# Optimization experiments

Measured on AMD Instinct MI355X. Metric: run time of the kernel, lower is better.

## Reference

```python
import jax, jax.numpy as jnp
import numpy as np

N = 100000        # nodes
E = 1600000       # edges (before self loops)
F_IN = 14         # Mutagenicity num_node_features
H = 64            # hidden_channels
C = 2             # Mutagenicity num_classes
G = 512           # graphs in batch
NEG_SLOPE = 0.2   # GATConv default leaky slope for attention logits


def setup_inputs() -> dict:
    key = jax.random.key(0)
    ks = jax.random.split(key, 40)
    inp = {
        "x": jax.random.normal(ks[0], (N, F_IN), jnp.float32),
        "edge_index": jax.random.randint(ks[1], (2, E), 0, N, dtype=jnp.int64),
        "batch": jnp.sort(jax.random.randint(ks[2], (N,), 0, G, dtype=jnp.int64)),
    }
    dims = [F_IN, H, H, H, H]
    ki = 3
    for l in range(5):
        fin = dims[l]
        s = 1.0 / np.sqrt(fin)
        inp[f"W{l}"] = jax.random.uniform(ks[ki], (fin, H), jnp.float32, -s, s); ki += 1
        inp[f"a_src{l}"] = jax.random.uniform(ks[ki], (H,), jnp.float32, -0.3, 0.3); ki += 1
        inp[f"a_dst{l}"] = jax.random.uniform(ks[ki], (H,), jnp.float32, -0.3, 0.3); ki += 1
        inp[f"b{l}"] = jnp.zeros((H,), jnp.float32)
    s = 1.0 / np.sqrt(H)
    inp["lin_W"] = jax.random.uniform(ks[ki], (H, C), jnp.float32, -s, s); ki += 1
    inp["lin_b"] = jnp.zeros((C,), jnp.float32)
    return inp


def _gat_layer(x, src, dst, W, a_s, a_d, b):
    # GATConv (heads=1): h = x W; e_ij = LeakyReLU(a_s.h_j + a_d.h_i);
    # alpha = softmax over incoming edges of node i; out_i = sum_j alpha_ij h_j + b
    h = x @ W                                   # [N, H]
    logit_s = h @ a_s                           # [N]
    logit_d = h @ a_d                           # [N]
    e = jax.nn.leaky_relu(logit_s[src] + logit_d[dst], NEG_SLOPE)  # [Etot]
    m = jax.ops.segment_max(e, dst, num_segments=N)
    m = jnp.where(jnp.isfinite(m), m, 0.0)      # empty segments -> 0 (none after self loops)
    ex = jnp.exp(e - m[dst])
    den = jax.ops.segment_sum(ex, dst, num_segments=N)
    alpha = ex / den[dst]                       # self loops guarantee den > 0
    out = jax.ops.segment_sum(alpha[:, None] * h[src], dst, num_segments=N)
    return out + b


def reference(x, edge_index, batch,
              W0, a_src0, a_dst0, b0,
              W1, a_src1, a_dst1, b1,
              W2, a_src2, a_dst2, b2,
              W3, a_src3, a_dst3, b3,
              W4, a_src4, a_dst4, b4,
              lin_W, lin_b):
    # add self loops once (GATConv default add_self_loops=True)
    loop = jnp.arange(N, dtype=edge_index.dtype)
    src = jnp.concatenate([edge_index[0], loop])
    dst = jnp.concatenate([edge_index[1], loop])

    h = x
    layers = [(W0, a_src0, a_dst0, b0), (W1, a_src1, a_dst1, b1),
              (W2, a_src2, a_dst2, b2), (W3, a_src3, a_dst3, b3),
              (W4, a_src4, a_dst4, b4)]
    for (W, a_s, a_d, b) in layers:
        h = jax.nn.elu(_gat_layer(h, src, dst, W, a_s, a_d, b))

    # global max pool over graphs
    g = jax.ops.segment_max(h, batch, num_segments=G)   # [G, H]
    g = jnp.where(jnp.isfinite(g), g, 0.0)
    return g @ lin_W + lin_b                             # [G, C]
```

## Files before the change

kernel.cpp:

```cpp
#include <hip/hip_runtime.h>
#include <hip/hip_fp16.h>
#include <math.h>

#define N_NODES 100000
#define H_DIM 64
#define G_GRAPHS 512
#define NEG_SLOPE 0.2f

#define BSHIFT 9
#define NBKT ((N_NODES + (1 << BSHIFT) - 1) >> BSHIFT)
#define CHUNK_E 4096

#define DEG_CAP 128

#define PK_SRC(v)  ((v) & 0x1FFFF)
#define PK_LD(v)   ((v) >> 17)


__global__ __launch_bounds__(256) void bucket_hist_kernel(const int* __restrict__ dst,
                                                          int* __restrict__ bcount, int E) {
    __shared__ int lh[NBKT];
    int t = threadIdx.x;
    for (int i = t; i < NBKT; i += 256) lh[i] = 0;
    __syncthreads();
    int base = blockIdx.x * CHUNK_E;
#pragma unroll
    for (int k = 0; k < 16; ++k) {
        int e = base + k * 256 + t;
        if (e < E) atomicAdd(&lh[dst[e] >> BSHIFT], 1);
    }
    __syncthreads();
    for (int i = t; i < NBKT; i += 256) {
        int c = lh[i];
        if (c) atomicAdd(&bcount[i], c);
    }
}

__global__ __launch_bounds__(256) void bucket_scan_kernel(const int* __restrict__ bcount,
                                                          int* __restrict__ bbase,
                                                          int* __restrict__ bfill,
                                                          int* __restrict__ off, int n) {
    __shared__ int sm[256];
    int t = threadIdx.x;
    sm[t] = (t < NBKT) ? bcount[t] : 0;
    __syncthreads();
    for (int d = 1; d < 256; d <<= 1) {
        int v = (t >= d) ? sm[t - d] : 0;
        __syncthreads();
        sm[t] += v;
        __syncthreads();
    }
    if (t < NBKT) {
        int ex = (t == 0) ? 0 : sm[t - 1];
        bbase[t] = ex;
        bfill[t] = ex;
    }
    if (t == 0) {
        bbase[NBKT] = sm[255];
        off[n] = sm[255];
    }
}

__global__ __launch_bounds__(256) void partition_kernel(const int* __restrict__ src,
                                                        const int* __restrict__ dst,
                                                        int* __restrict__ bfill,
                                                        int* __restrict__ ebuck, int E) {
    __shared__ int lh[NBKT];
    __shared__ int lbase[NBKT];
    int t = threadIdx.x;
    int base = blockIdx.x * CHUNK_E;
    for (int i = t; i < NBKT; i += 256) lh[i] = 0;
    __syncthreads();

    int pk[16], bk[16];
#pragma unroll
    for (int k = 0; k < 16; ++k) {
        int e = base + k * 256 + t;
        if (e < E) {
            int s = src[e];
            int d = dst[e];
            bk[k] = d >> BSHIFT;
            pk[k] = s | ((d & ((1 << BSHIFT) - 1)) << 17);
            atomicAdd(&lh[bk[k]], 1);
        } else {
            bk[k] = -1;
        }
    }
    __syncthreads();
    for (int i = t; i < NBKT; i += 256) {
        int c = lh[i];
        lbase[i] = c ? atomicAdd(&bfill[i], c) : 0;
        lh[i] = 0;
    }
    __syncthreads();
#pragma unroll
    for (int k = 0; k < 16; ++k) {
        if (bk[k] >= 0) {
            int r = atomicAdd(&lh[bk[k]], 1);
            ebuck[lbase[bk[k]] + r] = pk[k];
        }
    }
}

__global__ __launch_bounds__(256) void bucket_csr_kernel(const int* __restrict__ ebuck,
                                                         const int* __restrict__ bbase,
                                                         int* __restrict__ off,
                                                         int* __restrict__ esrc, int n) {
    __shared__ int cnt[512];
    __shared__ int loff[512];
    __shared__ int sm[256];
    int b = blockIdx.x;
    int t = threadIdx.x;
    int ebeg = bbase[b];
    int eend = bbase[b + 1];
    int nbeg = b << BSHIFT;
    int nloc = n - nbeg; if (nloc > 512) nloc = 512;

    cnt[t] = 0; cnt[t + 256] = 0;
    __syncthreads();
    for (int e = ebeg + t; e < eend; e += 256) {
        atomicAdd(&cnt[PK_LD(ebuck[e])], 1);
    }
    __syncthreads();
    int c0 = cnt[2 * t], c1 = cnt[2 * t + 1];
    sm[t] = c0 + c1;
    __syncthreads();
    for (int d = 1; d < 256; d <<= 1) {
        int v = (t >= d) ? sm[t - d] : 0;
        __syncthreads();
        sm[t] += v;
        __syncthreads();
    }
    int basep = (t == 0) ? 0 : sm[t - 1];
    loff[2 * t] = basep;
    loff[2 * t + 1] = basep + c0;
    cnt[2 * t] = 0; cnt[2 * t + 1] = 0;
    __syncthreads();
    for (int i = t; i < nloc; i += 256) off[nbeg + i] = ebeg + loff[i];
    for (int e = ebeg + t; e < eend; e += 256) {
        int v = ebuck[e];
        int d = PK_LD(v);
        int r = atomicAdd(&cnt[d], 1);
        esrc[ebeg + loff[d] + r] = PK_SRC(v);
    }
}

template <int FIN, int FINP, int XSTR>
__global__ __launch_bounds__(256) void gemm_tile_kernel(
        const float* __restrict__ act, const float* __restrict__ W,
        const float* __restrict__ a_s, const float* __restrict__ a_d,
        __half* __restrict__ h16,
        float* __restrict__ ls, float* __restrict__ ld,
        int n) {
    __shared__ float sx[128 * XSTR];
    __shared__ float sw[FINP * 64];
    int t = threadIdx.x;
    int tb = blockIdx.x * 128;
    int nrow = n - tb; if (nrow > 128) nrow = 128;

    {
        const float4* Wv = (const float4*)W;
        float4* swv = (float4*)sw;
        for (int i = t; i < FINP * 16; i += 256) {
            int k = i >> 4;
            swv[i] = (k < FIN) ? Wv[i] : make_float4(0.0f, 0.0f, 0.0f, 0.0f);
        }
    }
    if (FIN == 64) {
        for (int i = t; i < 128 * 16; i += 256) {
            int r = i >> 4, c4 = i & 15;
            float4 v = make_float4(0.0f, 0.0f, 0.0f, 0.0f);
            if (r < nrow) v = *(const float4*)(act + (size_t)(tb + r) * 64 + c4 * 4);
            *(float4*)(sx + r * XSTR + c4 * 4) = v;
        }
    } else {
        int c = t & 15;
        for (int r = t >> 4; r < 128; r += 16) {
            float v = 0.0f;
            if (r < nrow && c < FIN) v = act[(size_t)(tb + r) * FIN + c];
            sx[r * XSTR + c] = v;
        }
    }
    __syncthreads();

    int f4 = t & 15;
    int ng = t >> 4;

    float4 acc[8];
#pragma unroll
    for (int i = 0; i < 8; ++i) acc[i] = make_float4(0.0f, 0.0f, 0.0f, 0.0f);

    for (int k4 = 0; k4 < FINP; k4 += 4) {
        float4 w0 = *(const float4*)(sw + (k4 + 0) * 64 + f4 * 4);
        float4 w1 = *(const float4*)(sw + (k4 + 1) * 64 + f4 * 4);
        float4 w2 = *(const float4*)(sw + (k4 + 2) * 64 + f4 * 4);
        float4 w3 = *(const float4*)(sw + (k4 + 3) * 64 + f4 * 4);
#pragma unroll
        for (int i = 0; i < 8; ++i) {
            float4 xv = *(const float4*)(sx + (ng + 16 * i) * XSTR + k4);
            acc[i].x = fmaf(xv.x, w0.x, acc[i].x);
            acc[i].y = fmaf(xv.x, w0.y, acc[i].y);
            acc[i].z = fmaf(xv.x, w0.z, acc[i].z);
            acc[i].w = fmaf(xv.x, w0.w, acc[i].w);
            acc[i].x = fmaf(xv.y, w1.x, acc[i].x);
            acc[i].y = fmaf(xv.y, w1.y, acc[i].y);
            acc[i].z = fmaf(xv.y, w1.z, acc[i].z);
            acc[i].w = fmaf(xv.y, w1.w, acc[i].w);
            acc[i].x = fmaf(xv.z, w2.x, acc[i].x);
            acc[i].y = fmaf(xv.z, w2.y, acc[i].y);
            acc[i].z = fmaf(xv.z, w2.z, acc[i].z);
            acc[i].w = fmaf(xv.z, w2.w, acc[i].w);
            acc[i].x = fmaf(xv.w, w3.x, acc[i].x);
            acc[i].y = fmaf(xv.w, w3.y, acc[i].y);
            acc[i].z = fmaf(xv.w, w3.z, acc[i].z);
            acc[i].w = fmaf(xv.w, w3.w, acc[i].w);
        }
    }

    float4 as4 = *(const float4*)(a_s + f4 * 4);
    float4 ad4 = *(const float4*)(a_d + f4 * 4);
#pragma unroll
    for (int i = 0; i < 8; ++i) {
        int r = ng + 16 * i;
        if (r < nrow) {
            int node = tb + r;
            __half2 plo = __floats2half2_rn(acc[i].x, acc[i].y);
            __half2 phi = __floats2half2_rn(acc[i].z, acc[i].w);
            uint2 pk;
            pk.x = *reinterpret_cast<unsigned*>(&plo);
            pk.y = *reinterpret_cast<unsigned*>(&phi);
            *reinterpret_cast<uint2*>(h16 + (size_t)node * 64 + f4 * 4) = pk;
            float vs = acc[i].x * as4.x + acc[i].y * as4.y +
                       acc[i].z * as4.z + acc[i].w * as4.w;
            float vd = acc[i].x * ad4.x + acc[i].y * ad4.y +
                       acc[i].z * ad4.z + acc[i].w * ad4.w;
            vs += __shfl_xor(vs, 1, 64); vd += __shfl_xor(vd, 1, 64);
            vs += __shfl_xor(vs, 2, 64); vd += __shfl_xor(vd, 2, 64);
            vs += __shfl_xor(vs, 4, 64); vd += __shfl_xor(vd, 4, 64);
            vs += __shfl_xor(vs, 8, 64); vd += __shfl_xor(vd, 8, 64);
            if (f4 == 0) { ls[node] = vs; ld[node] = vd; }
        }
    }
}

__global__ __launch_bounds__(256) void gat_aggregate_kernel(
        const __half* __restrict__ h16,
        const float* __restrict__ ls,
        const float* __restrict__ ld, const int* __restrict__ off,
        const int* __restrict__ esrc, const float* __restrict__ bias,
        float* __restrict__ hout, int n) {
    __shared__ int2 smq[16 * DEG_CAP];
    int t = threadIdx.x;
    int fl = t & 15;
    int g = t >> 4;
    int node = blockIdx.x * 16 + g;
    if (node >= n) return;
    int2* sq = smq + g * DEG_CAP;
    int fl4 = fl * 4;

    int jb = off[node];
    int je = off[node + 1];
    int deg = je - jb;
    int degc = (deg < DEG_CAP) ? deg : DEG_CAP;
    float ldv = ld[node];
    float lself = ls[node];

    float mm = lself;
    for (int c = fl; c < degc; c += 16) {
        int s = esrc[jb + c];
        float v = ls[s];
        sq[c] = make_int2(s, __float_as_int(v));
        mm = fmaxf(mm, v);
    }
    for (int c = degc + fl; c < deg; c += 16) {
        mm = fmaxf(mm, ls[esrc[jb + c]]);
    }
    mm = fmaxf(mm, __shfl_xor(mm, 8, 64));
    mm = fmaxf(mm, __shfl_xor(mm, 4, 64));
    mm = fmaxf(mm, __shfl_xor(mm, 2, 64));
    mm = fmaxf(mm, __shfl_xor(mm, 1, 64));
    float mraw = mm + ldv;
    float m = (mraw >= 0.0f) ? mraw : NEG_SLOPE * mraw;

    float denl = 0.0f;
    for (int c = fl; c < degc; c += 16) {
        float e = __int_as_float(sq[c].y) + ldv;
        e = (e >= 0.0f) ? e : NEG_SLOPE * e;
        float p = __expf(e - m);
        sq[c].y = __float_as_int(p);
        denl += p;
    }
    int degc4 = (degc + 3) & ~3;
    if (fl < degc4 - degc) sq[degc + fl] = make_int2(node, 0);

    denl += __shfl_xor(denl, 8, 64);
    denl += __shfl_xor(denl, 4, 64);
    denl += __shfl_xor(denl, 2, 64);
    denl += __shfl_xor(denl, 1, 64);

    uint2 qs = *reinterpret_cast<const uint2*>(h16 + (size_t)node * 64 + fl4);
    float2 sa = __half22float2(*reinterpret_cast<__half2*>(&qs.x));
    float2 sb = __half22float2(*reinterpret_cast<__half2*>(&qs.y));

    float4 acc = make_float4(0.0f, 0.0f, 0.0f, 0.0f);
    for (int c = 0; c < degc4; c += 4) {
        int2 e0 = sq[c + 0];
        int2 e1 = sq[c + 1];
        int2 e2 = sq[c + 2];
        int2 e3 = sq[c + 3];
        uint2 q0 = *reinterpret_cast<const uint2*>(h16 + (size_t)e0.x * 64 + fl4);
        uint2 q1 = *reinterpret_cast<const uint2*>(h16 + (size_t)e1.x * 64 + fl4);
        uint2 q2 = *reinterpret_cast<const uint2*>(h16 + (size_t)e2.x * 64 + fl4);
        uint2 q3 = *reinterpret_cast<const uint2*>(h16 + (size_t)e3.x * 64 + fl4);
        float p0 = __int_as_float(e0.y), p1 = __int_as_float(e1.y);
        float p2 = __int_as_float(e2.y), p3 = __int_as_float(e3.y);
        float2 a0 = __half22float2(*reinterpret_cast<__half2*>(&q0.x));
        float2 b0 = __half22float2(*reinterpret_cast<__half2*>(&q0.y));
        float2 a1 = __half22float2(*reinterpret_cast<__half2*>(&q1.x));
        float2 b1 = __half22float2(*reinterpret_cast<__half2*>(&q1.y));
        float2 a2 = __half22float2(*reinterpret_cast<__half2*>(&q2.x));
        float2 b2 = __half22float2(*reinterpret_cast<__half2*>(&q2.y));
        float2 a3 = __half22float2(*reinterpret_cast<__half2*>(&q3.x));
        float2 b3 = __half22float2(*reinterpret_cast<__half2*>(&q3.y));
        acc.x = fmaf(p0, a0.x, acc.x); acc.y = fmaf(p0, a0.y, acc.y);
        acc.z = fmaf(p0, b0.x, acc.z); acc.w = fmaf(p0, b0.y, acc.w);
        acc.x = fmaf(p1, a1.x, acc.x); acc.y = fmaf(p1, a1.y, acc.y);
        acc.z = fmaf(p1, b1.x, acc.z); acc.w = fmaf(p1, b1.y, acc.w);
        acc.x = fmaf(p2, a2.x, acc.x); acc.y = fmaf(p2, a2.y, acc.y);
        acc.z = fmaf(p2, b2.x, acc.z); acc.w = fmaf(p2, b2.y, acc.w);
        acc.x = fmaf(p3, a3.x, acc.x); acc.y = fmaf(p3, a3.y, acc.y);
        acc.z = fmaf(p3, b3.x, acc.z); acc.w = fmaf(p3, b3.y, acc.w);
    }

    float den_of = 0.0f;
    for (int j = jb + DEG_CAP; j < je; ++j) {
        int s = esrc[j];
        float e = ls[s] + ldv;
        e = (e >= 0.0f) ? e : NEG_SLOPE * e;
        float p = __expf(e - m);
        den_of += p;
        uint2 qv = *reinterpret_cast<const uint2*>(h16 + (size_t)s * 64 + fl4);
        float2 va = __half22float2(*reinterpret_cast<__half2*>(&qv.x));
        float2 vb = __half22float2(*reinterpret_cast<__half2*>(&qv.y));
        acc.x = fmaf(p, va.x, acc.x);
        acc.y = fmaf(p, va.y, acc.y);
        acc.z = fmaf(p, vb.x, acc.z);
        acc.w = fmaf(p, vb.y, acc.w);
    }

    float e0s = lself + ldv;
    e0s = (e0s >= 0.0f) ? e0s : NEG_SLOPE * e0s;
    float p0s = __expf(e0s - m);
    float den = denl + den_of + p0s;
    acc.x = fmaf(p0s, sa.x, acc.x);
    acc.y = fmaf(p0s, sa.y, acc.y);
    acc.z = fmaf(p0s, sb.x, acc.z);
    acc.w = fmaf(p0s, sb.y, acc.w);

    const float4 b4 = *(const float4*)(bias + fl4);
    float inv = 1.0f / den;
    float4 o;
    o.x = acc.x * inv + b4.x;
    o.y = acc.y * inv + b4.y;
    o.z = acc.z * inv + b4.z;
    o.w = acc.w * inv + b4.w;
    o.x = (o.x > 0.0f) ? o.x : expm1f(o.x);
    o.y = (o.y > 0.0f) ? o.y : expm1f(o.y);
    o.z = (o.z > 0.0f) ? o.z : expm1f(o.z);
    o.w = (o.w > 0.0f) ? o.w : expm1f(o.w);
    *(float4*)(hout + (size_t)node * 64 + fl4) = o;
}

__device__ __forceinline__ unsigned enc_f32(float f) {
    unsigned b = __float_as_uint(f);
    return (b & 0x80000000u) ? ~b : (b | 0x80000000u);
}

__global__ __launch_bounds__(256) void pool_kernel(const float* __restrict__ h,
                                                   const int* __restrict__ batch,
                                                   unsigned* __restrict__ genc, int n) {
    int lane = threadIdx.x & 63;
    int w = blockIdx.x * 4 + (threadIdx.x >> 6);
    int start = w * 64;
    if (start >= n) return;
    int end = start + 64; if (end > n) end = n;
    int cur = batch[start];
    float rm = -1e38f;
    for (int node = start; node < end; ++node) {
        int b = batch[node];
        if (b != cur) {
            atomicMax(&genc[cur * 64 + lane], enc_f32(rm));
            cur = b;
            rm = -1e38f;
        }
        rm = fmaxf(rm, h[(size_t)node * 64 + lane]);
    }
    atomicMax(&genc[cur * 64 + lane], enc_f32(rm));
}

__global__ __launch_bounds__(64) void final_kernel(const unsigned* __restrict__ genc,
                                                   const float* __restrict__ linW,
                                                   const float* __restrict__ linb,
                                                   float* __restrict__ out) {
    int g = blockIdx.x;
    int lane = threadIdx.x;
    unsigned u = genc[g * 64 + lane];
    float v;
    if (u == 0u) {
        v = 0.0f;
    } else {
        unsigned b = (u & 0x80000000u) ? (u ^ 0x80000000u) : ~u;
        v = __uint_as_float(b);
    }
    float c0 = v * linW[lane * 2 + 0];
    float c1 = v * linW[lane * 2 + 1];
#pragma unroll
    for (int d = 32; d >= 1; d >>= 1) {
        c0 += __shfl_xor(c0, d, 64);
        c1 += __shfl_xor(c1, d, 64);
    }
    if (lane == 0) {
        out[g * 2 + 0] = c0 + linb[0];
        out[g * 2 + 1] = c1 + linb[1];
    }
}

static inline size_t align_up(size_t v, size_t a) { return (v + a - 1) & ~(a - 1); }

extern "C" void kernel_launch(void* const* d_in, const int* in_sizes, int n_in,
                              void* d_out, int out_size, void* d_ws, size_t ws_size,
                              hipStream_t stream) {
    const float* x          = (const float*)d_in[0];
    const int*   edge_index = (const int*)d_in[1];
    const int*   batch      = (const int*)d_in[2];
    const float* W[5];
    const float* a_s[5];
    const float* a_d[5];
    const float* bias[5];
    for (int l = 0; l < 5; ++l) {
        W[l]    = (const float*)d_in[3 + 4 * l + 0];
        a_s[l]  = (const float*)d_in[3 + 4 * l + 1];
        a_d[l]  = (const float*)d_in[3 + 4 * l + 2];
        bias[l] = (const float*)d_in[3 + 4 * l + 3];
    }
    const float* linW = (const float*)d_in[23];
    const float* linb = (const float*)d_in[24];
    float* out = (float*)d_out;

    const int N = N_NODES;
    const int E = in_sizes[1] / 2;
    const int* srcp = edge_index;
    const int* dstp = edge_index + E;

    char* p = (char*)d_ws;
    int* bcount = (int*)p;        p += align_up((size_t)NBKT * 4, 256);
    int* bbase  = (int*)p;        p += align_up((size_t)(NBKT + 1) * 4, 256);
    int* bfill  = (int*)p;        p += align_up((size_t)NBKT * 4, 256);
    int* off    = (int*)p;        p += align_up((size_t)(N + 1) * 4, 256);
    int* esrc   = (int*)p;        p += align_up((size_t)E * 4, 256);
    float* lsb  = (float*)p;      p += align_up((size_t)N * 4, 256);
    float* ldb  = (float*)p;      p += align_up((size_t)N * 4, 256);
    float* h_a  = (float*)p;      p += align_up((size_t)N * 64 * 4, 256);
    __half* h16 = (__half*)p;     p += align_up((size_t)N * 64 * 2, 256);
    unsigned* genc = (unsigned*)p; p += align_up((size_t)G_GRAPHS * 64 * 4, 256);

    int* ebuck = (int*)h_a;

    hipMemsetAsync(bcount, 0, (size_t)NBKT * 4, stream);
    hipMemsetAsync(genc, 0, (size_t)G_GRAPHS * 64 * 4, stream);

    int pb2 = (E + CHUNK_E - 1) / CHUNK_E;
    bucket_hist_kernel<<<pb2, 256, 0, stream>>>(dstp, bcount, E);
    bucket_scan_kernel<<<1, 256, 0, stream>>>(bcount, bbase, bfill, off, N);
    partition_kernel<<<pb2, 256, 0, stream>>>(srcp, dstp, bfill, ebuck, E);
    bucket_csr_kernel<<<NBKT, 256, 0, stream>>>(ebuck, bbase, off, esrc, N);

    int nb = (N + 15) / 16;
    int gt = (N + 127) / 128;
    gemm_tile_kernel<14, 16, 20><<<gt, 256, 0, stream>>>(x, W[0], a_s[0], a_d[0],
                                                         h16, lsb, ldb, N);
    gat_aggregate_kernel<<<nb, 256, 0, stream>>>(h16, lsb, ldb, off, esrc,
                                                 bias[0], h_a, N);
    for (int l = 1; l < 5; ++l) {
        gemm_tile_kernel<64, 64, 68><<<gt, 256, 0, stream>>>(h_a, W[l], a_s[l], a_d[l],
                                                             h16, lsb, ldb, N);
        gat_aggregate_kernel<<<nb, 256, 0, stream>>>(h16, lsb, ldb, off, esrc,
                                                     bias[l], h_a, N);
    }

    int pw = (N + 63) / 64;
    int pbk = (pw + 3) / 4;
    pool_kernel<<<pbk, 256, 0, stream>>>(h_a, batch, genc, N);
    final_kernel<<<G_GRAPHS, 64, 0, stream>>>(genc, linW, linb, out);
}
```

Before: 488.6 us.

## Fuse next-layer GEMM and attention logits into GAT aggregation epilogue

Each aggregation kernel now applies bias and ELU, then multiplies the result by the next layer's weight matrix held in shared memory, using wave shuffles to broadcast the row. It writes the fp16 features and the source and destination logits for the next layer directly, with ping-pong buffers. This removes four separate GEMM launches and the fp32 round trip of the 100000x64 activation through global memory. In exchange the aggregation kernel needs an extra 16KB of shared memory and more registers, which may reduce occupancy of a gather-bound kernel. A dedicated final kernel handles the last layer.

```diff
diff --git a/kernel.cpp b/kernel.cpp
--- a/kernel.cpp
+++ b/kernel.cpp
@@ -149,7 +149,7 @@
 __global__ __launch_bounds__(256) void gemm_tile_kernel(
         const float* __restrict__ act, const float* __restrict__ W,
         const float* __restrict__ a_s, const float* __restrict__ a_d,
-        __half* __restrict__ h16,
+        __half* __restrict__ h16g,
         float* __restrict__ ls, float* __restrict__ ld,
         int n) {
     __shared__ float sx[128 * XSTR];
@@ -166,14 +166,7 @@
             swv[i] = (k < FIN) ? Wv[i] : make_float4(0.0f, 0.0f, 0.0f, 0.0f);
         }
     }
-    if (FIN == 64) {
-        for (int i = t; i < 128 * 16; i += 256) {
-            int r = i >> 4, c4 = i & 15;
-            float4 v = make_float4(0.0f, 0.0f, 0.0f, 0.0f);
-            if (r < nrow) v = *(const float4*)(act + (size_t)(tb + r) * 64 + c4 * 4);
-            *(float4*)(sx + r * XSTR + c4 * 4) = v;
-        }
-    } else {
+    {
         int c = t & 15;
         for (int r = t >> 4; r < 128; r += 16) {
             float v = 0.0f;
@@ -229,7 +222,7 @@
             uint2 pk;
             pk.x = *reinterpret_cast<unsigned*>(&plo);
             pk.y = *reinterpret_cast<unsigned*>(&phi);
-            *reinterpret_cast<uint2*>(h16 + (size_t)node * 64 + f4 * 4) = pk;
+            *reinterpret_cast<uint2*>(h16g + (size_t)node * 64 + f4 * 4) = pk;
             float vs = acc[i].x * as4.x + acc[i].y * as4.y +
                        acc[i].z * as4.z + acc[i].w * as4.w;
             float vd = acc[i].x * ad4.x + acc[i].y * ad4.y +
@@ -243,14 +236,25 @@
     }
 }
 
-__global__ __launch_bounds__(256) void gat_aggregate_kernel(
-        const __half* __restrict__ h16,
-        const float* __restrict__ ls,
-        const float* __restrict__ ld, const int* __restrict__ off,
+__global__ __launch_bounds__(256) void gat_gemm_kernel(
+        const __half* __restrict__ h16_in, const float* __restrict__ ls_in,
+        const float* __restrict__ ld_in, const int* __restrict__ off,
         const int* __restrict__ esrc, const float* __restrict__ bias,
-        float* __restrict__ hout, int n) {
+        const float* __restrict__ Wn, const float* __restrict__ asn,
+        const float* __restrict__ adn,
+        __half* __restrict__ h16_out, float* __restrict__ ls_out,
+        float* __restrict__ ld_out, int n) {
+    __shared__ float sw[64 * 64];
     __shared__ int2 smq[16 * DEG_CAP];
     int t = threadIdx.x;
+    {
+        const float4* Wv = (const float4*)Wn;
+        float4* swv = (float4*)sw;
+        for (int i = t; i < 64 * 16; i += 256) swv[i] = Wv[i];
+    }
+    __syncthreads();
+
+    int lane = t & 63;
     int fl = t & 15;
     int g = t >> 4;
     int node = blockIdx.x * 16 + g;
@@ -262,18 +266,18 @@
     int je = off[node + 1];
     int deg = je - jb;
     int degc = (deg < DEG_CAP) ? deg : DEG_CAP;
-    float ldv = ld[node];
-    float lself = ls[node];
+    float ldv = ld_in[node];
+    float lself = ls_in[node];
 
     float mm = lself;
     for (int c = fl; c < degc; c += 16) {
         int s = esrc[jb + c];
-        float v = ls[s];
+        float v = ls_in[s];
         sq[c] = make_int2(s, __float_as_int(v));
         mm = fmaxf(mm, v);
     }
     for (int c = degc + fl; c < deg; c += 16) {
-        mm = fmaxf(mm, ls[esrc[jb + c]]);
+        mm = fmaxf(mm, ls_in[esrc[jb + c]]);
     }
     mm = fmaxf(mm, __shfl_xor(mm, 8, 64));
     mm = fmaxf(mm, __shfl_xor(mm, 4, 64));
@@ -298,7 +302,7 @@
     denl += __shfl_xor(denl, 2, 64);
     denl += __shfl_xor(denl, 1, 64);
 
-    uint2 qs = *reinterpret_cast<const uint2*>(h16 + (size_t)node * 64 + fl4);
+    uint2 qs = *reinterpret_cast<const uint2*>(h16_in + (size_t)node * 64 + fl4);
     float2 sa = __half22float2(*reinterpret_cast<__half2*>(&qs.x));
     float2 sb = __half22float2(*reinterpret_cast<__half2*>(&qs.y));
 
@@ -308,10 +312,10 @@
         int2 e1 = sq[c + 1];
         int2 e2 = sq[c + 2];
         int2 e3 = sq[c + 3];
-        uint2 q0 = *reinterpret_cast<const uint2*>(h16 + (size_t)e0.x * 64 + fl4);
-        uint2 q1 = *reinterpret_cast<const uint2*>(h16 + (size_t)e1.x * 64 + fl4);
-        uint2 q2 = *reinterpret_cast<const uint2*>(h16 + (size_t)e2.x * 64 + fl4);
-        uint2 q3 = *reinterpret_cast<const uint2*>(h16 + (size_t)e3.x * 64 + fl4);
+        uint2 q0 = *reinterpret_cast<const uint2*>(h16_in + (size_t)e0.x * 64 + fl4);
+        uint2 q1 = *reinterpret_cast<const uint2*>(h16_in + (size_t)e1.x * 64 + fl4);
+        uint2 q2 = *reinterpret_cast<const uint2*>(h16_in + (size_t)e2.x * 64 + fl4);
+        uint2 q3 = *reinterpret_cast<const uint2*>(h16_in + (size_t)e3.x * 64 + fl4);
         float p0 = __int_as_float(e0.y), p1 = __int_as_float(e1.y);
         float p2 = __int_as_float(e2.y), p3 = __int_as_float(e3.y);
         float2 a0 = __half22float2(*reinterpret_cast<__half2*>(&q0.x));
@@ -335,11 +339,178 @@
     float den_of = 0.0f;
     for (int j = jb + DEG_CAP; j < je; ++j) {
         int s = esrc[j];
-        float e = ls[s] + ldv;
+        float e = ls_in[s] + ldv;
         e = (e >= 0.0f) ? e : NEG_SLOPE * e;
         float p = __expf(e - m);
         den_of += p;
-        uint2 qv = *reinterpret_cast<const uint2*>(h16 + (size_t)s * 64 + fl4);
+        uint2 qv = *reinterpret_cast<const uint2*>(h16_in + (size_t)s * 64 + fl4);
+        float2 va = __half22float2(*reinterpret_cast<__half2*>(&qv.x));
+        float2 vb = __half22float2(*reinterpret_cast<__half2*>(&qv.y));
+        acc.x = fmaf(p, va.x, acc.x);
+        acc.y = fmaf(p, va.y, acc.y);
+        acc.z = fmaf(p, vb.x, acc.z);
+        acc.w = fmaf(p, vb.y, acc.w);
+    }
+
+    float e0s = lself + ldv;
+    e0s = (e0s >= 0.0f) ? e0s : NEG_SLOPE * e0s;
+    float p0s = __expf(e0s - m);
+    float den = denl + den_of + p0s;
+    acc.x = fmaf(p0s, sa.x, acc.x);
+    acc.y = fmaf(p0s, sa.y, acc.y);
+    acc.z = fmaf(p0s, sb.x, acc.z);
+    acc.w = fmaf(p0s, sb.y, acc.w);
+
+    const float4 b4 = *(const float4*)(bias + fl4);
+    float inv = 1.0f / den;
+    float4 o;
+    o.x = acc.x * inv + b4.x;
+    o.y = acc.y * inv + b4.y;
+    o.z = acc.z * inv + b4.z;
+    o.w = acc.w * inv + b4.w;
+    o.x = (o.x > 0.0f) ? o.x : expm1f(o.x);
+    o.y = (o.y > 0.0f) ? o.y : expm1f(o.y);
+    o.z = (o.z > 0.0f) ? o.z : expm1f(o.z);
+    o.w = (o.w > 0.0f) ? o.w : expm1f(o.w);
+
+    float4 ha = make_float4(0.0f, 0.0f, 0.0f, 0.0f);
+    int gb = lane & 48;
+#pragma unroll
+    for (int kk = 0; kk < 16; ++kk) {
+        float ox = __shfl(o.x, gb + kk, 64);
+        float oy = __shfl(o.y, gb + kk, 64);
+        float oz = __shfl(o.z, gb + kk, 64);
+        float ow = __shfl(o.w, gb + kk, 64);
+        const float4 w0 = *(const float4*)(sw + (4 * kk + 0) * 64 + fl4);
+        const float4 w1 = *(const float4*)(sw + (4 * kk + 1) * 64 + fl4);
+        const float4 w2 = *(const float4*)(sw + (4 * kk + 2) * 64 + fl4);
+        const float4 w3 = *(const float4*)(sw + (4 * kk + 3) * 64 + fl4);
+        ha.x = fmaf(ox, w0.x, ha.x); ha.y = fmaf(ox, w0.y, ha.y);
+        ha.z = fmaf(ox, w0.z, ha.z); ha.w = fmaf(ox, w0.w, ha.w);
+        ha.x = fmaf(oy, w1.x, ha.x); ha.y = fmaf(oy, w1.y, ha.y);
+        ha.z = fmaf(oy, w1.z, ha.z); ha.w = fmaf(oy, w1.w, ha.w);
+        ha.x = fmaf(oz, w2.x, ha.x); ha.y = fmaf(oz, w2.y, ha.y);
+        ha.z = fmaf(oz, w2.z, ha.z); ha.w = fmaf(oz, w2.w, ha.w);
+        ha.x = fmaf(ow, w3.x, ha.x); ha.y = fmaf(ow, w3.y, ha.y);
+        ha.z = fmaf(ow, w3.z, ha.z); ha.w = fmaf(ow, w3.w, ha.w);
+    }
+
+    {
+        __half2 plo = __floats2half2_rn(ha.x, ha.y);
+        __half2 phi = __floats2half2_rn(ha.z, ha.w);
+        uint2 pk;
+        pk.x = *reinterpret_cast<unsigned*>(&plo);
+        pk.y = *reinterpret_cast<unsigned*>(&phi);
+        *reinterpret_cast<uint2*>(h16_out + (size_t)node * 64 + fl4) = pk;
+    }
+    float4 as4 = *(const float4*)(asn + fl4);
+    float4 ad4 = *(const float4*)(adn + fl4);
+    float vs = ha.x * as4.x + ha.y * as4.y + ha.z * as4.z + ha.w * as4.w;
+    float vd = ha.x * ad4.x + ha.y * ad4.y + ha.z * ad4.z + ha.w * ad4.w;
+    vs += __shfl_xor(vs, 1, 64); vd += __shfl_xor(vd, 1, 64);
+    vs += __shfl_xor(vs, 2, 64); vd += __shfl_xor(vd, 2, 64);
+    vs += __shfl_xor(vs, 4, 64); vd += __shfl_xor(vd, 4, 64);
+    vs += __shfl_xor(vs, 8, 64); vd += __shfl_xor(vd, 8, 64);
+    if (fl == 0) { ls_out[node] = vs; ld_out[node] = vd; }
+}
+
+__global__ __launch_bounds__(256) void gat_final_kernel(
+        const __half* __restrict__ h16_in,
+        const float* __restrict__ ls_in,
+        const float* __restrict__ ld_in, const int* __restrict__ off,
+        const int* __restrict__ esrc, const float* __restrict__ bias,
+        float* __restrict__ hout, int n) {
+    __shared__ int2 smq[16 * DEG_CAP];
+    int t = threadIdx.x;
+    int fl = t & 15;
+    int g = t >> 4;
+    int node = blockIdx.x * 16 + g;
+    if (node >= n) return;
+    int2* sq = smq + g * DEG_CAP;
+    int fl4 = fl * 4;
+
+    int jb = off[node];
+    int je = off[node + 1];
+    int deg = je - jb;
+    int degc = (deg < DEG_CAP) ? deg : DEG_CAP;
+    float ldv = ld_in[node];
+    float lself = ls_in[node];
+
+    float mm = lself;
+    for (int c = fl; c < degc; c += 16) {
+        int s = esrc[jb + c];
+        float v = ls_in[s];
+        sq[c] = make_int2(s, __float_as_int(v));
+        mm = fmaxf(mm, v);
+    }
+    for (int c = degc + fl; c < deg; c += 16) {
+        mm = fmaxf(mm, ls_in[esrc[jb + c]]);
+    }
+    mm = fmaxf(mm, __shfl_xor(mm, 8, 64));
+    mm = fmaxf(mm, __shfl_xor(mm, 4, 64));
+    mm = fmaxf(mm, __shfl_xor(mm, 2, 64));
+    mm = fmaxf(mm, __shfl_xor(mm, 1, 64));
+    float mraw = mm + ldv;
+    float m = (mraw >= 0.0f) ? mraw : NEG_SLOPE * mraw;
+
+    float denl = 0.0f;
+    for (int c = fl; c < degc; c += 16) {
+        float e = __int_as_float(sq[c].y) + ldv;
+        e = (e >= 0.0f) ? e : NEG_SLOPE * e;
+        float p = __expf(e - m);
+        sq[c].y = __float_as_int(p);
+        denl += p;
+    }
+    int degc4 = (degc + 3) & ~3;
+    if (fl < degc4 - degc) sq[degc + fl] = make_int2(node, 0);
+
+    denl += __shfl_xor(denl, 8, 64);
+    denl += __shfl_xor(denl, 4, 64);
+    denl += __shfl_xor(denl, 2, 64);
+    denl += __shfl_xor(denl, 1, 64);
+
+    uint2 qs = *reinterpret_cast<const uint2*>(h16_in + (size_t)node * 64 + fl4);
+    float2 sa = __half22float2(*reinterpret_cast<__half2*>(&qs.x));
+    float2 sb = __half22float2(*reinterpret_cast<__half2*>(&qs.y));
+
+    float4 acc = make_float4(0.0f, 0.0f, 0.0f, 0.0f);
+    for (int c = 0; c < degc4; c += 4) {
+        int2 e0 = sq[c + 0];
+        int2 e1 = sq[c + 1];
+        int2 e2 = sq[c + 2];
+        int2 e3 = sq[c + 3];
+        uint2 q0 = *reinterpret_cast<const uint2*>(h16_in + (size_t)e0.x * 64 + fl4);
+        uint2 q1 = *reinterpret_cast<const uint2*>(h16_in + (size_t)e1.x * 64 + fl4);
+        uint2 q2 = *reinterpret_cast<const uint2*>(h16_in + (size_t)e2.x * 64 + fl4);
+        uint2 q3 = *reinterpret_cast<const uint2*>(h16_in + (size_t)e3.x * 64 + fl4);
+        float p0 = __int_as_float(e0.y), p1 = __int_as_float(e1.y);
+        float p2 = __int_as_float(e2.y), p3 = __int_as_float(e3.y);
+        float2 a0 = __half22float2(*reinterpret_cast<__half2*>(&q0.x));
+        float2 b0 = __half22float2(*reinterpret_cast<__half2*>(&q0.y));
+        float2 a1 = __half22float2(*reinterpret_cast<__half2*>(&q1.x));
+        float2 b1 = __half22float2(*reinterpret_cast<__half2*>(&q1.y));
+        float2 a2 = __half22float2(*reinterpret_cast<__half2*>(&q2.x));
+        float2 b2 = __half22float2(*reinterpret_cast<__half2*>(&q2.y));
+        float2 a3 = __half22float2(*reinterpret_cast<__half2*>(&q3.x));
+        float2 b3 = __half22float2(*reinterpret_cast<__half2*>(&q3.y));
+        acc.x = fmaf(p0, a0.x, acc.x); acc.y = fmaf(p0, a0.y, acc.y);
+        acc.z = fmaf(p0, b0.x, acc.z); acc.w = fmaf(p0, b0.y, acc.w);
+        acc.x = fmaf(p1, a1.x, acc.x); acc.y = fmaf(p1, a1.y, acc.y);
+        acc.z = fmaf(p1, b1.x, acc.z); acc.w = fmaf(p1, b1.y, acc.w);
+        acc.x = fmaf(p2, a2.x, acc.x); acc.y = fmaf(p2, a2.y, acc.y);
+        acc.z = fmaf(p2, b2.x, acc.z); acc.w = fmaf(p2, b2.y, acc.w);
+        acc.x = fmaf(p3, a3.x, acc.x); acc.y = fmaf(p3, a3.y, acc.y);
+        acc.z = fmaf(p3, b3.x, acc.z); acc.w = fmaf(p3, b3.y, acc.w);
+    }
+
+    float den_of = 0.0f;
+    for (int j = jb + DEG_CAP; j < je; ++j) {
+        int s = esrc[j];
+        float e = ls_in[s] + ldv;
+        e = (e >= 0.0f) ? e : NEG_SLOPE * e;
+        float p = __expf(e - m);
+        den_of += p;
+        uint2 qv = *reinterpret_cast<const uint2*>(h16_in + (size_t)s * 64 + fl4);
         float2 va = __half22float2(*reinterpret_cast<__half2*>(&qv.x));
         float2 vb = __half22float2(*reinterpret_cast<__half2*>(&qv.y));
         acc.x = fmaf(p, va.x, acc.x);
@@ -458,10 +629,13 @@
     int* bfill  = (int*)p;        p += align_up((size_t)NBKT * 4, 256);
     int* off    = (int*)p;        p += align_up((size_t)(N + 1) * 4, 256);
     int* esrc   = (int*)p;        p += align_up((size_t)E * 4, 256);
-    float* lsb  = (float*)p;      p += align_up((size_t)N * 4, 256);
-    float* ldb  = (float*)p;      p += align_up((size_t)N * 4, 256);
+    float* lsA  = (float*)p;      p += align_up((size_t)N * 4, 256);
+    float* ldA  = (float*)p;      p += align_up((size_t)N * 4, 256);
+    float* lsB  = (float*)p;      p += align_up((size_t)N * 4, 256);
+    float* ldB  = (float*)p;      p += align_up((size_t)N * 4, 256);
+    __half* h16A = (__half*)p;    p += align_up((size_t)N * 64 * 2, 256);
+    __half* h16B = (__half*)p;    p += align_up((size_t)N * 64 * 2, 256);
     float* h_a  = (float*)p;      p += align_up((size_t)N * 64 * 4, 256);
-    __half* h16 = (__half*)p;     p += align_up((size_t)N * 64 * 2, 256);
     unsigned* genc = (unsigned*)p; p += align_up((size_t)G_GRAPHS * 64 * 4, 256);
 
     int* ebuck = (int*)h_a;
@@ -477,16 +651,23 @@
 
     int nb = (N + 15) / 16;
     int gt = (N + 127) / 128;
-    gemm_tile_kernel<14, 16, 20><<<gt, 256, 0, stream>>>(x, W[0], a_s[0], a_d[0],
-                                                         h16, lsb, ldb, N);
-    gat_aggregate_kernel<<<nb, 256, 0, stream>>>(h16, lsb, ldb, off, esrc,
-                                                 bias[0], h_a, N);
-    for (int l = 1; l < 5; ++l) {
-        gemm_tile_kernel<64, 64, 68><<<gt, 256, 0, stream>>>(h_a, W[l], a_s[l], a_d[l],
-                                                             h16, lsb, ldb, N);
-        gat_aggregate_kernel<<<nb, 256, 0, stream>>>(h16, lsb, ldb, off, esrc,
-                                                     bias[l], h_a, N);
-    }
+
+    gemm_tile_kernel<14, 16, 20><<<gt, 256, 0, stream>>>(
+        x, W[0], a_s[0], a_d[0], h16A, lsA, ldA, N);
+    gat_gemm_kernel<<<nb, 256, 0, stream>>>(
+        h16A, lsA, ldA, off, esrc, bias[0], W[1], a_s[1], a_d[1],
+        h16B, lsB, ldB, N);
+    gat_gemm_kernel<<<nb, 256, 0, stream>>>(
+        h16B, lsB, ldB, off, esrc, bias[1], W[2], a_s[2], a_d[2],
+        h16A, lsA, ldA, N);
+    gat_gemm_kernel<<<nb, 256, 0, stream>>>(
+        h16A, lsA, ldA, off, esrc, bias[2], W[3], a_s[3], a_d[3],
+        h16B, lsB, ldB, N);
+    gat_gemm_kernel<<<nb, 256, 0, stream>>>(
+        h16B, lsB, ldB, off, esrc, bias[3], W[4], a_s[4], a_d[4],
+        h16A, lsA, ldA, N);
+    gat_final_kernel<<<nb, 256, 0, stream>>>(
+        h16A, lsA, ldA, off, esrc, bias[4], h_a, N);
 
     int pw = (N + 63) / 64;
     int pbk = (pw + 3) / 4;
```

After: 502.0 us. +2.7%, slower.
